# Kernel optimization log

Measured on AMD Instinct MI355X. Metric: run time of the kernel, lower is better.

Reference implementation:

```python
import jax, jax.numpy as jnp
import numpy as np

IM_H = 256.0
IM_W = 256.0


def setup_inputs() -> dict:
    key = jax.random.key(0)
    k1, k2 = jax.random.split(key)
    feats = jax.random.normal(k1, (8, 64, 64, 64), dtype=jnp.float32)
    Kcam = jax.random.normal(k2, (2, 4, 3, 4), dtype=jnp.float32)
    vmax = jnp.ones((2, 3), dtype=jnp.float32)
    vmin = jnp.zeros((2, 3), dtype=jnp.float32)
    return {"feats": feats, "Kcam": Kcam, "vmax": vmax, "vmin": vmin, "nvox": 48}


def reference(feats, Kcam, vmax, vmin, nvox):
    nR, fdim, fh, fw = feats.shape
    batch, view = Kcam.shape[0], Kcam.shape[1]
    rsz_h = float(fh) / IM_H
    rsz_w = float(fw) / IM_W

    # Build voxel grid per batch: linspace(vmin, vmax, nvox) along each axis.
    t = jnp.linspace(0.0, 1.0, nvox, dtype=jnp.float32)  # [nvox]
    rng = vmin[:, :, None] + (vmax - vmin)[:, :, None] * t  # [batch, 3, nvox]
    shp = (batch, nvox, nvox, nvox)
    gx = jnp.broadcast_to(rng[:, 0, :, None, None], shp)  # meshgrid 'ij' (torch default)
    gy = jnp.broadcast_to(rng[:, 1, None, :, None], shp)
    gz = jnp.broadcast_to(rng[:, 2, None, None, :], shp)
    grid = jnp.stack([gx, gy, gz], axis=1).reshape(batch, 3, -1)  # [batch, 3, nV]
    nV = grid.shape[2]
    rs_grid = jnp.concatenate([grid, jnp.ones((batch, 1, nV), jnp.float32)], axis=1)  # [batch, 4, nV]

    # Perspective projection: [batch, view*3, 4] @ [batch, 4, nV]
    im_p = jnp.einsum('bvrk,bkn->bvrn', Kcam, rs_grid).reshape(batch * view, 3, nV)
    im_x, im_y, im_z = im_p[:, 0, :], im_p[:, 1, :], im_p[:, 2, :]
    im_x = jnp.clip(im_x / im_z * rsz_w, 0.0, fw - 1)
    im_y = jnp.clip(im_y / im_z * rsz_h, 0.0, fh - 1)

    im_x0 = jnp.floor(im_x)
    im_x1 = jnp.clip(im_x0 + 1.0, 0.0, fw - 1)
    im_y0 = jnp.floor(im_y)
    im_y1 = jnp.clip(im_y0 + 1.0, 0.0, fh - 1)

    flat = feats.reshape(nR, fdim, fh * fw)  # [nR, fdim, fh*fw]

    def gather(xi, yi):
        idx = (yi * fw + xi).astype(jnp.int32)  # [nR, nV]
        return jax.vmap(lambda f, i: f[:, i])(flat, idx)  # [nR, fdim, nV]

    Ia = gather(im_x0, im_y0)
    Ib = gather(im_x0, im_y1)
    Ic = gather(im_x1, im_y0)
    Id = gather(im_x1, im_y1)

    wa = ((im_x1 - im_x) * (im_y1 - im_y))[:, None, :]
    wb = ((im_x1 - im_x) * (im_y - im_y0))[:, None, :]
    wc = ((im_x - im_x0) * (im_y1 - im_y))[:, None, :]
    wd = ((im_x - im_x0) * (im_y - im_y0))[:, None, :]

    Ibilin = wa * Ia + wb * Ib + wc * Ic + wd * Id  # [nR, fdim, nV]
    return Ibilin.reshape(nR, fdim, nvox, nvox, nvox)
```

## Files before the change

### kernel.cpp

```cpp
#include <hip/hip_runtime.h>


#define NR    8
#define FDIM  64
#define FH    64
#define FW    64
#define IMG   (FH * FW)
#define NVOX  48
#define NV    (NVOX * NVOX * NVOX)
#define THREADS 256
#define QUARTERS 4
#define VPB   (NV / QUARTERS)
#define ITERS (VPB / THREADS)

typedef float f32x4 __attribute__((ext_vector_type(4)));

__global__ __launch_bounds__(THREADS, 4) void proj_splat_kernel(
    const float* __restrict__ feats,
    const float* __restrict__ Kcam,
    const float* __restrict__ vmax,
    const float* __restrict__ vmin,
    float* __restrict__ out)
{
    __shared__ float lds[2 * IMG + 1];

    const int t  = threadIdx.x;
    const int cp = blockIdx.x;
    const int qq = blockIdx.y;
    const int r  = blockIdx.z;
    const int b  = r >> 2;

    const float* src = feats + ((size_t)r * FDIM + 2 * cp) * IMG;
#pragma unroll
    for (int q = 0; q < 8; ++q) {
        const int off = q * (THREADS * 4) + t * 4;
        *reinterpret_cast<f32x4*>(&lds[off]) =
            *reinterpret_cast<const f32x4*>(src + off);
    }
    if (t == 0) lds[2 * IMG] = 0.0f;
    __syncthreads();

    const float inv = 1.0f / (float)(NVOX - 1);
    const float* vmn = vmin + b * 3;
    const float* vmx = vmax + b * 3;
    const float ax = (vmx[0] - vmn[0]) * inv;
    const float ay = (vmx[1] - vmn[1]) * inv;
    const float az = (vmx[2] - vmn[2]) * inv;
    const float* K = Kcam + r * 12;
    const float A0 = K[0] * ax, B0 = K[1] * ay, D0 = K[2]  * az;
    const float C0 = K[0] * vmn[0] + K[1] * vmn[1] + K[2]  * vmn[2] + K[3];
    const float A1 = K[4] * ax, B1 = K[5] * ay, D1 = K[6]  * az;
    const float C1 = K[4] * vmn[0] + K[5] * vmn[1] + K[6]  * vmn[2] + K[7];
    const float A2 = K[8] * ax, B2 = K[9] * ay, D2 = K[10] * az;
    const float C2 = K[8] * vmn[0] + K[9] * vmn[1] + K[10] * vmn[2] + K[11];

    float* o0 = out + ((size_t)r * FDIM + 2 * cp) * NV;
    float* o1 = o0 + NV;

    int n = qq * VPB + t;
    int i = n / (NVOX * NVOX);
    int j = (n / NVOX) % NVOX;
    int k = n % NVOX;

    for (int it = 0; it < ITERS; ++it) {
        const float fi = (float)i, fj = (float)j, fk = (float)k;
        const float px = C0 + A0 * fi + B0 * fj + D0 * fk;
        const float py = C1 + A1 * fi + B1 * fj + D1 * fk;
        const float pz = C2 + A2 * fi + B2 * fj + D2 * fk;

        const float rz = 0.25f / pz;
        float imx = px * rz;
        float imy = py * rz;
        imx = fminf(fmaxf(imx, 0.0f), (float)(FW - 1));
        imy = fminf(fmaxf(imy, 0.0f), (float)(FH - 1));

        const float x0 = floorf(imx);
        const float x1 = fminf(x0 + 1.0f, (float)(FW - 1));
        const float y0 = floorf(imy);
        const float y1 = fminf(y0 + 1.0f, (float)(FH - 1));

        const float wa = (x1 - imx) * (y1 - imy);
        const float wc = (imx - x0) * (y1 - imy);
        const float wb = (x1 - imx) * (imy - y0);
        const float wd = (imx - x0) * (imy - y0);

        const int ix0 = (int)x0;
        const int iy0 = (int)y0;
        const int iy1 = (int)y1;
        const int ia = iy0 * FW + ix0;
        const int ib = iy1 * FW + ix0;

        {
            const float a0 = lds[ia],       a1 = lds[ia + 1];
            const float b0 = lds[ib],       b1 = lds[ib + 1];
            const float res = wa * a0 + wc * a1 + wb * b0 + wd * b1;
            __builtin_nontemporal_store(res, o0 + n);
        }
        {
            const float a0 = lds[IMG + ia], a1 = lds[IMG + ia + 1];
            const float b0 = lds[IMG + ib], b1 = lds[IMG + ib + 1];
            const float res = wa * a0 + wc * a1 + wb * b0 + wd * b1;
            __builtin_nontemporal_store(res, o1 + n);
        }

        n += THREADS;
        k += 16;
        if (k >= NVOX) { k -= NVOX; j += 6; } else { j += 5; }
        if (j >= NVOX) { j -= NVOX; i += 1; }
    }
}

extern "C" void kernel_launch(void* const* d_in, const int* in_sizes, int n_in,
                              void* d_out, int out_size, void* d_ws, size_t ws_size,
                              hipStream_t stream) {
    const float* feats = (const float*)d_in[0];
    const float* Kcam  = (const float*)d_in[1];
    const float* vmax  = (const float*)d_in[2];
    const float* vmin  = (const float*)d_in[3];
    float* out = (float*)d_out;

    dim3 grid(FDIM / 2, QUARTERS, NR);
    dim3 block(THREADS);
    proj_splat_kernel<<<grid, block, 0, stream>>>(feats, Kcam, vmax, vmin, out);
}
```

Before: 242.9 us.

## Interleave four channels per texel in swizzled LDS and use 512-thread blocks

```diff
diff --git a/kernel.cpp b/kernel.cpp
--- a/kernel.cpp
+++ b/kernel.cpp
@@ -8,12 +8,16 @@
 #define IMG   (FH * FW)
 #define NVOX  48
 #define NV    (NVOX * NVOX * NVOX)
-#define THREADS 256
+#define THREADS 512
 #define QUARTERS 4
 #define VPB   (NV / QUARTERS)
 #define ITERS (VPB / THREADS)
 
 typedef float f32x4 __attribute__((ext_vector_type(4)));
+
+__device__ __forceinline__ int slotof(int y, int x) {
+    return (y << 6) + (x ^ (y & 7));
+}
 
 __global__ __launch_bounds__(THREADS, 4) void proj_splat_kernel(
     const float* __restrict__ feats,
@@ -22,22 +26,32 @@
     const float* __restrict__ vmin,
     float* __restrict__ out)
 {
-    __shared__ float lds[2 * IMG + 1];
+    __shared__ f32x4 lds4[IMG];
 
     const int t  = threadIdx.x;
-    const int cp = blockIdx.x;
+    const int cg = blockIdx.x;
     const int qq = blockIdx.y;
     const int r  = blockIdx.z;
     const int b  = r >> 2;
 
-    const float* src = feats + ((size_t)r * FDIM + 2 * cp) * IMG;
+    const float* s0 = feats + ((size_t)r * FDIM + cg * 4) * IMG;
+    const float* s1 = s0 + IMG;
+    const float* s2 = s1 + IMG;
+    const float* s3 = s2 + IMG;
 #pragma unroll
-    for (int q = 0; q < 8; ++q) {
-        const int off = q * (THREADS * 4) + t * 4;
-        *reinterpret_cast<f32x4*>(&lds[off]) =
-            *reinterpret_cast<const f32x4*>(src + off);
+    for (int q = 0; q < 2; ++q) {
+        const int i = q * 2048 + t * 4;
+        const int y = i >> 6, x = i & 63;
+        const f32x4 a  = *reinterpret_cast<const f32x4*>(s0 + i);
+        const f32x4 bb = *reinterpret_cast<const f32x4*>(s1 + i);
+        const f32x4 c  = *reinterpret_cast<const f32x4*>(s2 + i);
+        const f32x4 d  = *reinterpret_cast<const f32x4*>(s3 + i);
+#pragma unroll
+        for (int m = 0; m < 4; ++m) {
+            f32x4 v = { a[m], bb[m], c[m], d[m] };
+            lds4[slotof(y, x + m)] = v;
+        }
     }
-    if (t == 0) lds[2 * IMG] = 0.0f;
     __syncthreads();
 
     const float inv = 1.0f / (float)(NVOX - 1);
@@ -54,8 +68,10 @@
     const float A2 = K[8] * ax, B2 = K[9] * ay, D2 = K[10] * az;
     const float C2 = K[8] * vmn[0] + K[9] * vmn[1] + K[10] * vmn[2] + K[11];
 
-    float* o0 = out + ((size_t)r * FDIM + 2 * cp) * NV;
+    float* o0 = out + ((size_t)r * FDIM + cg * 4) * NV;
     float* o1 = o0 + NV;
+    float* o2 = o1 + NV;
+    float* o3 = o2 + NV;
 
     int n = qq * VPB + t;
     int i = n / (NVOX * NVOX);
@@ -84,28 +100,23 @@
         const float wb = (x1 - imx) * (imy - y0);
         const float wd = (imx - x0) * (imy - y0);
 
-        const int ix0 = (int)x0;
-        const int iy0 = (int)y0;
-        const int iy1 = (int)y1;
-        const int ia = iy0 * FW + ix0;
-        const int ib = iy1 * FW + ix0;
+        const int ix0 = (int)x0, ix1 = (int)x1;
+        const int iy0 = (int)y0, iy1 = (int)y1;
 
-        {
-            const float a0 = lds[ia],       a1 = lds[ia + 1];
-            const float b0 = lds[ib],       b1 = lds[ib + 1];
-            const float res = wa * a0 + wc * a1 + wb * b0 + wd * b1;
-            __builtin_nontemporal_store(res, o0 + n);
-        }
-        {
-            const float a0 = lds[IMG + ia], a1 = lds[IMG + ia + 1];
-            const float b0 = lds[IMG + ib], b1 = lds[IMG + ib + 1];
-            const float res = wa * a0 + wc * a1 + wb * b0 + wd * b1;
-            __builtin_nontemporal_store(res, o1 + n);
-        }
+        const f32x4 p00 = lds4[slotof(iy0, ix0)];
+        const f32x4 p01 = lds4[slotof(iy0, ix1)];
+        const f32x4 p10 = lds4[slotof(iy1, ix0)];
+        const f32x4 p11 = lds4[slotof(iy1, ix1)];
+
+        const f32x4 res = wa * p00 + wc * p01 + wb * p10 + wd * p11;
+        o0[n] = res.x;
+        o1[n] = res.y;
+        o2[n] = res.z;
+        o3[n] = res.w;
 
         n += THREADS;
-        k += 16;
-        if (k >= NVOX) { k -= NVOX; j += 6; } else { j += 5; }
+        k += 32;
+        if (k >= NVOX) { k -= NVOX; j += 11; } else { j += 10; }
         if (j >= NVOX) { j -= NVOX; i += 1; }
     }
 }
@@ -119,7 +130,7 @@
     const float* vmin  = (const float*)d_in[3];
     float* out = (float*)d_out;
 
-    dim3 grid(FDIM / 2, QUARTERS, NR);
+    dim3 grid(FDIM / 4, QUARTERS, NR);
     dim3 block(THREADS);
     proj_splat_kernel<<<grid, block, 0, stream>>>(feats, Kcam, vmax, vmin, out);
 }
```

Result: faster. 233.1 us (-4.0%).
